# Performance work log

Hardware: AMD Instinct MI355X
Metric: run time of the kernel (lower is better)

## Reference

```python
import jax, jax.numpy as jnp
import numpy as np

DIM = 768
B, H_DIM, W_DIM = 16, 64, 64
N = H_DIM * W_DIM
WEIGHT_BITS = 5
SHIFT_MIN = -(2 ** (WEIGHT_BITS - 1) - 2)  # -14
SHIFT_MAX = 0
INT_BITS, FRAC_BITS = 16, 16


def round_to_fixed(x):
    # DeepShift utils.round_to_fixed: floor-based fixed-point quantization
    delta = 2.0 ** (-FRAC_BITS)
    bound = 2.0 ** (INT_BITS - 1)
    return jnp.clip(jnp.floor(x / delta) * delta, -bound, bound - 1)


def setup_inputs() -> dict:
    key = jax.random.key(0)
    k1, k2, k3, k4 = jax.random.split(key, 4)
    x = jax.random.normal(k1, (B, N, DIM), dtype=jnp.float32)
    # shift / sign parameters of Conv2dShift, depthwise kernel [C, 1, 3, 3]
    shift = jax.random.uniform(k2, (DIM, 1, 3, 3), minval=float(SHIFT_MIN), maxval=0.0, dtype=jnp.float32)
    sign = jax.random.uniform(k3, (DIM, 1, 3, 3), minval=-1.0, maxval=1.0, dtype=jnp.float32)
    bias = jax.random.normal(k4, (DIM,), dtype=jnp.float32) * 0.01
    return {"x": x, "shift": shift, "sign": sign, "bias": bias, "H": H_DIM, "W": W_DIM}


def reference(x, shift, sign, bias, H, W):
    Bb, Nn, C = x.shape
    # weight = sign(round(sign_param)) * 2**round(clamp(shift, [-14, 0]))
    shift_r = jnp.round(jnp.clip(shift, SHIFT_MIN, SHIFT_MAX))
    sign_r = jnp.sign(jnp.round(sign))
    w = (2.0 ** shift_r) * sign_r  # [C, 1, 3, 3] power-of-two weights
    # fixed-point quantize activations and bias
    xq = round_to_fixed(x)
    bq = round_to_fixed(bias)
    # [B, N, C] -> [B, C, H, W]
    img = jnp.transpose(xq, (0, 2, 1)).reshape(Bb, C, H, W)
    out = jax.lax.conv_general_dilated(
        img, w,
        window_strides=(1, 1),
        padding=((1, 1), (1, 1)),
        dimension_numbers=("NCHW", "OIHW", "NCHW"),
        feature_group_count=C,
    )
    out = out + bq[None, :, None, None]
    # [B, C, H, W] -> [B, N, C]
    return jnp.transpose(out.reshape(Bb, C, Nn), (0, 2, 1))
```

## Files before the change

kernel.cpp:

```cpp
#include <hip/hip_runtime.h>


#define DIM 768
#define HD  64
#define WD  64
#define BD  16
#define TW  4
#define TH  16
#define NPIX (HD * WD)

typedef float f32x4 __attribute__((ext_vector_type(4)));

__device__ __forceinline__ float qfix(float x) {
    float v = floorf(x * 65536.0f) * 1.52587890625e-05f;
    return fminf(fmaxf(v, -32768.0f), 32767.0f);
}

__device__ __forceinline__ float4 zero4() { return make_float4(0.f, 0.f, 0.f, 0.f); }

__device__ __forceinline__ float4 q4(float4 v) {
    v.x = qfix(v.x); v.y = qfix(v.y); v.z = qfix(v.z); v.w = qfix(v.w);
    return v;
}

__device__ __forceinline__ float4 fma4(float4 a, float4 b, float4 c) {
    c.x = fmaf(a.x, b.x, c.x);
    c.y = fmaf(a.y, b.y, c.y);
    c.z = fmaf(a.z, b.z, c.z);
    c.w = fmaf(a.w, b.w, c.w);
    return c;
}

__global__ void wprep_kernel(const float* __restrict__ shift,
                             const float* __restrict__ sgn,
                             const float* __restrict__ bias,
                             float* __restrict__ wbuf,
                             float* __restrict__ bbuf) {
    int i = blockIdx.x * 256 + threadIdx.x;
    if (i < DIM * 9) {
        int c = i / 9;
        int k = i - c * 9;
        float sr = rintf(fminf(fmaxf(shift[i], -14.0f), 0.0f));
        float g  = rintf(sgn[i]);
        float sg = (g > 0.0f) ? 1.0f : ((g < 0.0f) ? -1.0f : 0.0f);
        wbuf[k * DIM + c] = exp2f(sr) * sg;
    }
    if (i < DIM) bbuf[i] = qfix(bias[i]);
}

__device__ __forceinline__ void load_row6(float4* r, const float* p,
                                          bool rowvalid, bool lv, bool rv) {
    #pragma unroll
    for (int j = 0; j < 6; ++j) {
        bool v = rowvalid && (j == 0 ? lv : (j == 5 ? rv : true));
        r[j] = v ? q4(*(const float4*)(p + (j - 1) * DIM)) : zero4();
    }
}

__global__ __launch_bounds__(192) void dwconv_kernel(
        const float* __restrict__ x,
        const float* __restrict__ wbuf,
        const float* __restrict__ bbuf,
        float* __restrict__ out) {
    const int c  = threadIdx.x * 4;
    const int w0 = blockIdx.x * TW;
    const int h0 = blockIdx.y * TH;
    const int b  = blockIdx.z;

    float4 wk[9];
    #pragma unroll
    for (int k = 0; k < 9; ++k)
        wk[k] = *(const float4*)(wbuf + k * DIM + c);
    const float4 bq = *(const float4*)(bbuf + c);

    const bool lv = (w0 > 0), rv = (w0 + TW < WD);
    const float* xb = x   + ((size_t)b * NPIX + w0) * DIM + c;
    float*       ob = out + ((size_t)b * NPIX + w0) * DIM + c;
    const long rowstride = (long)WD * DIM;

    float4 r0[6], r1[6], r2[6];
    load_row6(r0, xb + (long)(h0 - 1) * rowstride, h0 > 0, lv, rv);
    load_row6(r1, xb + (long)h0 * rowstride, true, lv, rv);

    #pragma unroll
    for (int hh = 0; hh < TH; ++hh) {
        const int h = h0 + hh;
        load_row6(r2, xb + (long)(h + 1) * rowstride, (h + 1) < HD, lv, rv);

        float4 acc[TW];
        #pragma unroll
        for (int i = 0; i < TW; ++i) acc[i] = bq;

        #pragma unroll
        for (int kx = 0; kx < 3; ++kx) {
            #pragma unroll
            for (int i = 0; i < TW; ++i) {
                acc[i] = fma4(wk[0 + kx], r0[i + kx], acc[i]);
                acc[i] = fma4(wk[3 + kx], r1[i + kx], acc[i]);
                acc[i] = fma4(wk[6 + kx], r2[i + kx], acc[i]);
            }
        }

        #pragma unroll
        for (int i = 0; i < TW; ++i) {
            f32x4 av;
            av.x = acc[i].x; av.y = acc[i].y; av.z = acc[i].z; av.w = acc[i].w;
            __builtin_nontemporal_store(av,
                (f32x4*)(ob + (long)h * rowstride + (long)i * DIM));
        }

        #pragma unroll
        for (int j = 0; j < 6; ++j) { r0[j] = r1[j]; r1[j] = r2[j]; }
    }
}

extern "C" void kernel_launch(void* const* d_in, const int* in_sizes, int n_in,
                              void* d_out, int out_size, void* d_ws, size_t ws_size,
                              hipStream_t stream) {
    const float* x     = (const float*)d_in[0];
    const float* shift = (const float*)d_in[1];
    const float* sgn   = (const float*)d_in[2];
    const float* bias  = (const float*)d_in[3];
    float* out  = (float*)d_out;
    float* wbuf = (float*)d_ws;
    float* bbuf = wbuf + 9 * DIM;

    wprep_kernel<<<(DIM * 9 + 255) / 256, 256, 0, stream>>>(shift, sgn, bias, wbuf, bbuf);

    dim3 grid(WD / TW, HD / TH, BD);
    dwconv_kernel<<<grid, 192, 0, stream>>>(x, wbuf, bbuf, out);
}
```

Baseline: 386.6 us.

## Halve row tile, prefetch rows one step ahead, and swizzle block order for XCDs

Cuts the row tile height from 16 to 8, which doubles the block count and adds halo re-reads. Uses a four-row register rotation so the next input row is loaded one iteration early, hiding load latency behind the FMAs. Remaps the linear block id so each group of eight consecutively dispatched blocks spreads across the chip, presumably to keep neighbouring tiles on the same XCD for L2 reuse. The trade-offs are more halo traffic and higher register pressure from the extra prefetch buffer.

```diff
diff --git a/kernel.cpp b/kernel.cpp
--- a/kernel.cpp
+++ b/kernel.cpp
@@ -6,8 +6,11 @@
 #define WD  64
 #define BD  16
 #define TW  4
-#define TH  16
+#define TH  8
 #define NPIX (HD * WD)
+#define NBX (WD / TW)
+#define NBY (HD / TH)
+#define NBLK (NBX * NBY * BD)
 
 typedef float f32x4 __attribute__((ext_vector_type(4)));
 
@@ -62,10 +65,16 @@
         const float* __restrict__ wbuf,
         const float* __restrict__ bbuf,
         float* __restrict__ out) {
+    int nbid = blockIdx.x + NBX * (blockIdx.y + NBY * blockIdx.z);
+    int swz  = (nbid & 7) * (NBLK / 8) + (nbid >> 3);
+    const int bx = swz % NBX; swz /= NBX;
+    const int by = swz % NBY; swz /= NBY;
+    const int bz = swz;
+
     const int c  = threadIdx.x * 4;
-    const int w0 = blockIdx.x * TW;
-    const int h0 = blockIdx.y * TH;
-    const int b  = blockIdx.z;
+    const int w0 = bx * TW;
+    const int h0 = by * TH;
+    const int b  = bz;
 
     float4 wk[9];
     #pragma unroll
@@ -78,14 +87,16 @@
     float*       ob = out + ((size_t)b * NPIX + w0) * DIM + c;
     const long rowstride = (long)WD * DIM;
 
-    float4 r0[6], r1[6], r2[6];
-    load_row6(r0, xb + (long)(h0 - 1) * rowstride, h0 > 0, lv, rv);
-    load_row6(r1, xb + (long)h0 * rowstride, true, lv, rv);
+    float4 A[6], B[6], C[6], D[6];
+    load_row6(A, xb + (long)(h0 - 1) * rowstride, h0 > 0, lv, rv);
+    load_row6(B, xb + (long)h0 * rowstride, true, lv, rv);
+    load_row6(C, xb + (long)(h0 + 1) * rowstride, (h0 + 1) < HD, lv, rv);
 
     #pragma unroll
     for (int hh = 0; hh < TH; ++hh) {
         const int h = h0 + hh;
-        load_row6(r2, xb + (long)(h + 1) * rowstride, (h + 1) < HD, lv, rv);
+        if (hh < TH - 1)
+            load_row6(D, xb + (long)(h + 2) * rowstride, (h + 2) < HD, lv, rv);
 
         float4 acc[TW];
         #pragma unroll
@@ -95,9 +106,9 @@
         for (int kx = 0; kx < 3; ++kx) {
             #pragma unroll
             for (int i = 0; i < TW; ++i) {
-                acc[i] = fma4(wk[0 + kx], r0[i + kx], acc[i]);
-                acc[i] = fma4(wk[3 + kx], r1[i + kx], acc[i]);
-                acc[i] = fma4(wk[6 + kx], r2[i + kx], acc[i]);
+                acc[i] = fma4(wk[0 + kx], A[i + kx], acc[i]);
+                acc[i] = fma4(wk[3 + kx], B[i + kx], acc[i]);
+                acc[i] = fma4(wk[6 + kx], C[i + kx], acc[i]);
             }
         }
 
@@ -110,7 +121,7 @@
         }
 
         #pragma unroll
-        for (int j = 0; j < 6; ++j) { r0[j] = r1[j]; r1[j] = r2[j]; }
+        for (int j = 0; j < 6; ++j) { A[j] = B[j]; B[j] = C[j]; C[j] = D[j]; }
     }
 }
 
@@ -127,6 +138,6 @@
 
     wprep_kernel<<<(DIM * 9 + 255) / 256, 256, 0, stream>>>(shift, sgn, bias, wbuf, bbuf);
 
-    dim3 grid(WD / TW, HD / TH, BD);
+    dim3 grid(NBX, NBY, BD);
     dwconv_kernel<<<grid, 192, 0, stream>>>(x, wbuf, bbuf, out);
 }
```

After: 364.4 us. 5.7% less time.

## Stage quantized input tiles in LDS with channel-sliced spatial blocks

Applied to the files above, without the earlier changes.

The depthwise conv now splits channels into 64-wide slices and spatial tiles of 16x8. Each block loads the haloed tile once, quantizes it, and stores it in LDS, then every thread computes one output column down 8 rows from shared memory. This cuts the redundant global re-reads of halo columns that the per-thread register sliding window had. It also adds a block-index swizzle meant to spread blocks across XCDs/L2. The cost is LDS traffic, a __syncthreads barrier with no overlap between load and compute, and a larger halo fraction per tile.

```diff
diff --git a/kernel.cpp b/kernel.cpp
--- a/kernel.cpp
+++ b/kernel.cpp
@@ -5,9 +5,16 @@
 #define HD  64
 #define WD  64
 #define BD  16
-#define TW  4
-#define TH  16
+#define CS  64
+#define NSL (DIM / CS)
+#define TLW 16
+#define TLH 8
 #define NPIX (HD * WD)
+#define LROWS (TLH + 2)
+#define LPX   (TLW + 2)
+#define STG_ELEMS (LROWS * LPX * (CS / 4))
+#define STG_ITERS ((STG_ELEMS + 255) / 256)
+#define NBLK (4 * 8 * NSL * BD)
 
 typedef float f32x4 __attribute__((ext_vector_type(4)));
 
@@ -16,18 +23,15 @@
     return fminf(fmaxf(v, -32768.0f), 32767.0f);
 }
 
-__device__ __forceinline__ float4 zero4() { return make_float4(0.f, 0.f, 0.f, 0.f); }
-
-__device__ __forceinline__ float4 q4(float4 v) {
-    v.x = qfix(v.x); v.y = qfix(v.y); v.z = qfix(v.z); v.w = qfix(v.w);
+__device__ __forceinline__ f32x4 q4v(f32x4 v) {
+    #pragma unroll
+    for (int i = 0; i < 4; ++i) v[i] = qfix(v[i]);
     return v;
 }
 
-__device__ __forceinline__ float4 fma4(float4 a, float4 b, float4 c) {
-    c.x = fmaf(a.x, b.x, c.x);
-    c.y = fmaf(a.y, b.y, c.y);
-    c.z = fmaf(a.z, b.z, c.z);
-    c.w = fmaf(a.w, b.w, c.w);
+__device__ __forceinline__ f32x4 fma4(f32x4 a, f32x4 b, f32x4 c) {
+    #pragma unroll
+    for (int i = 0; i < 4; ++i) c[i] = fmaf(a[i], b[i], c[i]);
     return c;
 }
 
@@ -48,69 +52,84 @@
     if (i < DIM) bbuf[i] = qfix(bias[i]);
 }
 
-__device__ __forceinline__ void load_row6(float4* r, const float* p,
-                                          bool rowvalid, bool lv, bool rv) {
-    #pragma unroll
-    for (int j = 0; j < 6; ++j) {
-        bool v = rowvalid && (j == 0 ? lv : (j == 5 ? rv : true));
-        r[j] = v ? q4(*(const float4*)(p + (j - 1) * DIM)) : zero4();
-    }
-}
-
-__global__ __launch_bounds__(192) void dwconv_kernel(
+__global__ __launch_bounds__(256, 3) void dwconv_kernel(
         const float* __restrict__ x,
         const float* __restrict__ wbuf,
         const float* __restrict__ bbuf,
         float* __restrict__ out) {
-    const int c  = threadIdx.x * 4;
-    const int w0 = blockIdx.x * TW;
-    const int h0 = blockIdx.y * TH;
-    const int b  = blockIdx.z;
+    __shared__ float lds[LROWS][LPX][CS];
 
-    float4 wk[9];
+    int nbid = blockIdx.x + 4 * (blockIdx.y + 8 * blockIdx.z);
+    int swz  = (nbid & 7) * (NBLK / 8) + (nbid >> 3);
+    const int bx = swz & 3;
+    const int by = (swz >> 2) & 7;
+    const int bz = swz >> 5;
+
+    const int tid  = threadIdx.x;
+    const int c4   = tid & 15;
+    const int wloc = tid >> 4;
+    const int w0 = bx * TLW, h0 = by * TLH;
+    const int cb = (bz % NSL) * CS;
+    const int b  = bz / NSL;
+
+    f32x4 tmp[STG_ITERS];
+    #pragma unroll
+    for (int k = 0; k < STG_ITERS; ++k) {
+        int idx = tid + k * 256;
+        if (idx < STG_ELEMS) {
+            int sc  = idx & 15;
+            int px  = (idx >> 4) % LPX;
+            int row = idx / (16 * LPX);
+            int h = h0 - 1 + row, w = w0 - 1 + px;
+            bool v = (h >= 0) & (h < HD) & (w >= 0) & (w < WD);
+            tmp[k] = v ? q4v(*(const f32x4*)(
+                         x + ((size_t)b * NPIX + (size_t)h * WD + w) * DIM
+                           + cb + sc * 4))
+                       : (f32x4)0.f;
+        }
+    }
+    #pragma unroll
+    for (int k = 0; k < STG_ITERS; ++k) {
+        int idx = tid + k * 256;
+        if (idx < STG_ELEMS) {
+            int sc  = idx & 15;
+            int px  = (idx >> 4) % LPX;
+            int row = idx / (16 * LPX);
+            *(f32x4*)&lds[row][px][sc * 4] = tmp[k];
+        }
+    }
+
+    f32x4 wk[9];
     #pragma unroll
     for (int k = 0; k < 9; ++k)
-        wk[k] = *(const float4*)(wbuf + k * DIM + c);
-    const float4 bq = *(const float4*)(bbuf + c);
+        wk[k] = *(const f32x4*)(wbuf + k * DIM + cb + c4 * 4);
+    const f32x4 bq = *(const f32x4*)(bbuf + cb + c4 * 4);
 
-    const bool lv = (w0 > 0), rv = (w0 + TW < WD);
-    const float* xb = x   + ((size_t)b * NPIX + w0) * DIM + c;
-    float*       ob = out + ((size_t)b * NPIX + w0) * DIM + c;
-    const long rowstride = (long)WD * DIM;
+    __syncthreads();
 
-    float4 r0[6], r1[6], r2[6];
-    load_row6(r0, xb + (long)(h0 - 1) * rowstride, h0 > 0, lv, rv);
-    load_row6(r1, xb + (long)h0 * rowstride, true, lv, rv);
-
+    f32x4 A[3], B[3], C[3];
     #pragma unroll
-    for (int hh = 0; hh < TH; ++hh) {
-        const int h = h0 + hh;
-        load_row6(r2, xb + (long)(h + 1) * rowstride, (h + 1) < HD, lv, rv);
-
-        float4 acc[TW];
+    for (int i = 0; i < 3; ++i) {
+        A[i] = *(const f32x4*)&lds[0][wloc + i][c4 * 4];
+        B[i] = *(const f32x4*)&lds[1][wloc + i][c4 * 4];
+    }
+    float* op = out + ((size_t)b * NPIX + (size_t)h0 * WD + w0 + wloc) * DIM
+                    + cb + c4 * 4;
+    #pragma unroll
+    for (int hh = 0; hh < TLH; ++hh) {
         #pragma unroll
-        for (int i = 0; i < TW; ++i) acc[i] = bq;
-
+        for (int i = 0; i < 3; ++i)
+            C[i] = *(const f32x4*)&lds[hh + 2][wloc + i][c4 * 4];
+        f32x4 acc = bq;
         #pragma unroll
-        for (int kx = 0; kx < 3; ++kx) {
-            #pragma unroll
-            for (int i = 0; i < TW; ++i) {
-                acc[i] = fma4(wk[0 + kx], r0[i + kx], acc[i]);
-                acc[i] = fma4(wk[3 + kx], r1[i + kx], acc[i]);
-                acc[i] = fma4(wk[6 + kx], r2[i + kx], acc[i]);
-            }
+        for (int i = 0; i < 3; ++i) {
+            acc = fma4(wk[i],     A[i], acc);
+            acc = fma4(wk[3 + i], B[i], acc);
+            acc = fma4(wk[6 + i], C[i], acc);
         }
-
+        __builtin_nontemporal_store(acc, (f32x4*)(op + (size_t)hh * WD * DIM));
         #pragma unroll
-        for (int i = 0; i < TW; ++i) {
-            f32x4 av;
-            av.x = acc[i].x; av.y = acc[i].y; av.z = acc[i].z; av.w = acc[i].w;
-            __builtin_nontemporal_store(av,
-                (f32x4*)(ob + (long)h * rowstride + (long)i * DIM));
-        }
-
-        #pragma unroll
-        for (int j = 0; j < 6; ++j) { r0[j] = r1[j]; r1[j] = r2[j]; }
+        for (int i = 0; i < 3; ++i) { A[i] = B[i]; B[i] = C[i]; }
     }
 }
 
@@ -127,6 +146,6 @@
 
     wprep_kernel<<<(DIM * 9 + 255) / 256, 256, 0, stream>>>(shift, sgn, bias, wbuf, bbuf);
 
-    dim3 grid(WD / TW, HD / TH, BD);
-    dwconv_kernel<<<grid, 192, 0, stream>>>(x, wbuf, bbuf, out);
+    dim3 grid(4, 8, NSL * BD);
+    dwconv_kernel<<<grid, 256, 0, stream>>>(x, wbuf, bbuf, out);
 }
```

Result: faster. 371.9 us (-3.8%).
